# Performance work log

Hardware: AMD Instinct MI355X
Metric: run time of the kernel (lower is better)

Reference implementation:

```python
import jax, jax.numpy as jnp
import numpy as np

N_CODES = 8192
CODE_DIM = 256
COMMITMENT_COST = 0.25
EMA_DECAY = 0.99
EPS = 1e-5


def setup_inputs() -> dict:
    key = jax.random.key(0)
    k1, k2 = jax.random.split(key)
    B, N, D, K = 8, 2048, CODE_DIM, N_CODES
    z = jax.random.normal(k1, (B, N, D), dtype=jnp.float32)
    # torch init: uniform(-1/n_codes, 1/n_codes); use small-scale init for realism
    emb_weight = jax.random.uniform(k2, (K, D), minval=-1.0 / K, maxval=1.0 / K, dtype=jnp.float32)
    return {
        "z": z,
        "emb_weight": emb_weight,
        "ema_cluster_size": jnp.zeros((K,), jnp.float32),
        "ema_w": jnp.zeros((K, D), jnp.float32),
        "code_usage": jnp.zeros((K,), jnp.float32),
    }


def reference(z, emb_weight, ema_cluster_size, ema_w, code_usage):
    # training=True path of VectorQuantizerV2.forward
    B, N, D = z.shape
    K = emb_weight.shape[0]
    z_flat = z.reshape(-1, D)  # [T, D], T = B*N

    # squared L2 distances: ||z||^2 + ||e||^2 - 2 z e^T  -> [T, K]
    d = (jnp.sum(z_flat * z_flat, axis=1, keepdims=True)
         + jnp.sum(emb_weight * emb_weight, axis=1)
         - 2.0 * z_flat @ emb_weight.T)
    idx = jnp.argmin(d, axis=-1)  # [T] int32

    z_q = emb_weight[idx].reshape(B, N, D)

    # usage tracking (scatter-add of ones == segment counts)
    cluster_size = jax.ops.segment_sum(jnp.ones_like(idx, jnp.float32), idx, num_segments=K)
    new_code_usage = code_usage + cluster_size

    # EMA codebook update (no one-hot materialization; segment_sum == encodings.T @ z)
    new_ecs = ema_cluster_size * EMA_DECAY + (1.0 - EMA_DECAY) * cluster_size
    n = jnp.sum(new_ecs)
    new_ecs = (new_ecs + EPS) / (n + K * EPS) * n  # Laplace smoothing
    dw = jax.ops.segment_sum(z_flat, idx, num_segments=K)  # [K, D]
    new_ema_w = ema_w * EMA_DECAY + (1.0 - EMA_DECAY) * dw
    new_emb_weight = new_ema_w / jnp.clip(new_ecs, EPS, None)[:, None]

    # losses (computed with z_q from the OLD codebook, matching torch op order)
    commitment_loss = jnp.mean((z - jax.lax.stop_gradient(z_q)) ** 2)
    codebook_loss = jnp.mean((z_q - jax.lax.stop_gradient(z)) ** 2)
    vq_loss = COMMITMENT_COST * commitment_loss + codebook_loss

    # straight-through estimator
    z_q_out = z + jax.lax.stop_gradient(z_q - z)

    # perplexity from empirical code distribution of this batch
    avg_probs = cluster_size / (B * N)
    perplexity = jnp.exp(-jnp.sum(avg_probs * jnp.log(avg_probs + 1e-10)))

    unique_codes = jnp.sum(new_code_usage > 0).astype(jnp.float32)
    usage_ratio = unique_codes / K

    indices = idx.reshape(B, N)
    return (z_q_out, indices, vq_loss, perplexity, usage_ratio, unique_codes,
            new_emb_weight, new_ecs, new_ema_w, new_code_usage)
```

## Files before the change

kernel.cpp:

```cpp
#include <hip/hip_runtime.h>
#include <hip/hip_bf16.h>
#include <math.h>

#define TOKS 16384
#define DDIM 256
#define KC   8192

static constexpr float EMA   = 0.99f;
static constexpr float ONE_M = (float)(1.0 - 0.99);
static constexpr float EPSF  = 1e-5f;
static constexpr float KEPS  = (float)(8192 * 1e-5);

#define CTILE  32
#define CAP    128
#define DELTA  2.0e-4f

#define CS_OFF    0
#define SCAL_OFF  8192
#define AN_OFF    8208
#define BN_OFF    24592
#define IDX_OFF   32784
#define CNT_OFF   49168
#define GMX_OFF   65552
#define THR0_OFF  81936
#define EB_OFF    98320
#define LISTS_OFF 1146896

typedef __attribute__((ext_vector_type(8))) short bf16x8;
typedef __attribute__((ext_vector_type(4))) short bf16x4;
typedef __attribute__((ext_vector_type(4))) float f32x4;

static __device__ inline short f2b(float f) {
  __hip_bfloat16 h = __float2bfloat16(f);
  return *reinterpret_cast<short*>(&h);
}
static __device__ inline unsigned int fkey(float f) {
  unsigned int b = __float_as_uint(f);
  return (b & 0x80000000u) ? ~b : (b | 0x80000000u);
}
static __device__ inline float funkey(unsigned int k) {
  unsigned int b = (k & 0x80000000u) ? (k & 0x7FFFFFFFu) : ~k;
  return __uint_as_float(b);
}

__global__ __launch_bounds__(256) void k_convbn(const float* __restrict__ e,
                                                unsigned short* __restrict__ eb,
                                                float* __restrict__ bn) {
  const int lane = threadIdx.x & 63;
  const int row = blockIdx.x * 4 + (threadIdx.x >> 6);
  const float4 v = *reinterpret_cast<const float4*>(e + (size_t)row * DDIM + lane * 4);
  bf16x4 b;
  b[0] = f2b(v.x); b[1] = f2b(v.y); b[2] = f2b(v.z); b[3] = f2b(v.w);
  *reinterpret_cast<bf16x4*>(eb + (size_t)row * DDIM + lane * 4) = b;
  float s = v.x * v.x + v.y * v.y + v.z * v.z + v.w * v.w;
#pragma unroll
  for (int d = 32; d; d >>= 1) s += __shfl_down(s, d);
  if (lane == 0) bn[row] = s;
}

__global__ __launch_bounds__(256) void k_convz(const float* __restrict__ z,
                                               unsigned short* __restrict__ zb,
                                               float* __restrict__ an) {
  const int lane = threadIdx.x & 63;
  const int row = blockIdx.x * 4 + (threadIdx.x >> 6);
  const float4 v = *reinterpret_cast<const float4*>(z + (size_t)row * DDIM + lane * 4);
  bf16x4 b;
  b[0] = f2b(v.x); b[1] = f2b(v.y); b[2] = f2b(v.z); b[3] = f2b(v.w);
  *reinterpret_cast<bf16x4*>(zb + (size_t)row * DDIM + lane * 4) = b;
  float s = v.x * v.x + v.y * v.y + v.z * v.z + v.w * v.w;
#pragma unroll
  for (int d = 32; d; d >>= 1) s += __shfl_down(s, d);
  if (lane == 0) an[row] = s;
}

template<bool COLLECT>
__global__ __launch_bounds__(256, 4) void k_screen(
    const unsigned short* __restrict__ zb, const unsigned short* __restrict__ eb,
    unsigned int* __restrict__ gmx, const float* __restrict__ thr0,
    unsigned int* __restrict__ cnt, unsigned short* __restrict__ lists) {
  constexpr int CHUNKC = COLLECT ? 1024 : 256;
  constexpr int NITC = CHUNKC / CTILE;
  __shared__ unsigned short Bt[2][CTILE * 256];

  const int tid = threadIdx.x;
  const int lane = tid & 63;
  const int w = tid >> 6;
  const int t0 = blockIdx.x * 128;
  const int k0 = blockIdx.y * CHUNKC;

  bf16x8 a[2][8];
  {
    const int rlo = lane & 15;
    const int khi = (lane >> 4) * 8;
#pragma unroll
    for (int rf = 0; rf < 2; ++rf) {
      const unsigned short* zr =
          zb + (size_t)(t0 + w * 32 + rf * 16 + rlo) * DDIM + khi;
#pragma unroll
      for (int kk = 0; kk < 8; ++kk)
        a[rf][kk] = *reinterpret_cast<const bf16x8*>(zr + kk * 32);
    }
  }

  float tr[2][4];
  float rm[2][4];
#pragma unroll
  for (int rf = 0; rf < 2; ++rf)
#pragma unroll
    for (int r = 0; r < 4; ++r) {
      rm[rf][r] = -1e30f;
      if (COLLECT) tr[rf][r] = thr0[t0 + w * 32 + rf * 16 + (lane >> 4) * 4 + r];
    }

  const char* ebB = reinterpret_cast<const char*>(eb);
  const int sc = tid >> 3;
  const int ss = tid & 7;
  const int swz = (sc & 7) << 4;

  {
    const size_t gb = (size_t)(k0 + sc) * 512 + ss * 16;
    char* dst = reinterpret_cast<char*>(&Bt[0][0]) + sc * 512;
#pragma unroll
    for (int q = 0; q < 4; ++q) {
      const uint4 g = *reinterpret_cast<const uint4*>(ebB + gb + q * 128);
      *reinterpret_cast<uint4*>(dst + ((ss * 16 + q * 128) ^ swz)) = g;
    }
  }
  __syncthreads();

  const int rdlo = lane & 15;
  const int rdhi = (lane >> 4) * 16;
  uint4 g[4];

  for (int ct = 0; ct < NITC; ++ct) {
    if (ct + 1 < NITC) {
      const size_t gb = (size_t)(k0 + (ct + 1) * CTILE + sc) * 512 + ss * 16;
#pragma unroll
      for (int q = 0; q < 4; ++q)
        g[q] = *reinterpret_cast<const uint4*>(ebB + gb + q * 128);
    }

    f32x4 acc[2][2];
#pragma unroll
    for (int rf = 0; rf < 2; ++rf)
#pragma unroll
      for (int cf = 0; cf < 2; ++cf) acc[rf][cf] = (f32x4){0.f, 0.f, 0.f, 0.f};

    const char* buf = reinterpret_cast<const char*>(&Bt[ct & 1][0]);
#pragma unroll
    for (int kk = 0; kk < 8; ++kk) {
      const int off = (kk * 64 + rdhi) ^ ((rdlo & 7) << 4);
      const bf16x8 b0 = *reinterpret_cast<const bf16x8*>(buf + rdlo * 512 + off);
      const bf16x8 b1 = *reinterpret_cast<const bf16x8*>(buf + (16 + rdlo) * 512 + off);
      acc[0][0] = __builtin_amdgcn_mfma_f32_16x16x32_bf16(a[0][kk], b0, acc[0][0], 0, 0, 0);
      acc[1][0] = __builtin_amdgcn_mfma_f32_16x16x32_bf16(a[1][kk], b0, acc[1][0], 0, 0, 0);
      acc[0][1] = __builtin_amdgcn_mfma_f32_16x16x32_bf16(a[0][kk], b1, acc[0][1], 0, 0, 0);
      acc[1][1] = __builtin_amdgcn_mfma_f32_16x16x32_bf16(a[1][kk], b1, acc[1][1], 0, 0, 0);
    }

    if (!COLLECT) {
#pragma unroll
      for (int rf = 0; rf < 2; ++rf)
#pragma unroll
        for (int r = 0; r < 4; ++r)
          rm[rf][r] = fmaxf(rm[rf][r], fmaxf(acc[rf][0][r], acc[rf][1][r]));
    } else {
      const int kb = k0 + ct * CTILE;
#pragma unroll
      for (int rf = 0; rf < 2; ++rf) {
#pragma unroll
        for (int r = 0; r < 4; ++r) {
          const float th = tr[rf][r];
          if (acc[rf][0][r] >= th || acc[rf][1][r] >= th) {
            const int t = t0 + w * 32 + rf * 16 + (lane >> 4) * 4 + r;
            if (acc[rf][0][r] >= th) {
              const unsigned int o_ = atomicAdd(&cnt[t], 1u);
              if (o_ < CAP) lists[(size_t)t * CAP + o_] = (unsigned short)(kb + rdlo);
            }
            if (acc[rf][1][r] >= th) {
              const unsigned int o_ = atomicAdd(&cnt[t], 1u);
              if (o_ < CAP) lists[(size_t)t * CAP + o_] = (unsigned short)(kb + 16 + rdlo);
            }
          }
        }
      }
    }

    if (ct + 1 < NITC) {
      char* dst = reinterpret_cast<char*>(&Bt[(ct + 1) & 1][0]) + sc * 512;
#pragma unroll
      for (int q = 0; q < 4; ++q)
        *reinterpret_cast<uint4*>(dst + ((ss * 16 + q * 128) ^ swz)) = g[q];
    }
    __syncthreads();
  }

  if (!COLLECT) {
#pragma unroll
    for (int rf = 0; rf < 2; ++rf) {
#pragma unroll
      for (int r = 0; r < 4; ++r) {
        float v = rm[rf][r];
#pragma unroll
        for (int o = 1; o <= 8; o <<= 1) v = fmaxf(v, __shfl_xor(v, o));
        if ((lane & 15) == 0) {
          const int t = t0 + w * 32 + rf * 16 + (lane >> 4) * 4 + r;
          atomicMax(&gmx[t], fkey(v));
        }
      }
    }
  }
}

__global__ __launch_bounds__(256) void k_thr(const unsigned int* __restrict__ gmx,
                                             float* __restrict__ thr) {
  const int t = blockIdx.x * 256 + threadIdx.x;
  thr[t] = funkey(gmx[t]) - DELTA;
}

__global__ __launch_bounds__(256) void k_rescore(
    const float* __restrict__ z, const float* __restrict__ emb,
    const float* __restrict__ an, const float* __restrict__ bn,
    const unsigned int* __restrict__ cnt, const unsigned short* __restrict__ lists,
    float* __restrict__ out_idx, int* __restrict__ idx_i) {
  const int w = threadIdx.x >> 6;
  const int lane = threadIdx.x & 63;
  const int t = blockIdx.x * 4 + w;

  const float4 z4 = *reinterpret_cast<const float4*>(z + (size_t)t * DDIM + lane * 4);
  const unsigned int nraw = cnt[t];
  const float aN = an[t];
  float bd = 3.4e38f;
  int bk = 0x7fffffff;

  if (nraw <= CAP) {
    const int n = (int)nraw;
    for (int c = 0; c < n; ++c) {
      const int k = (int)lists[(size_t)t * CAP + c];
      const float4 e4 = *reinterpret_cast<const float4*>(emb + (size_t)k * DDIM + lane * 4);
      float p = z4.x * e4.x + z4.y * e4.y + z4.z * e4.z + z4.w * e4.w;
#pragma unroll
      for (int o = 32; o; o >>= 1) p += __shfl_xor(p, o);
      const float d = __fsub_rn(__fadd_rn(aN, bn[k]), __fmul_rn(2.0f, p));
      if (d < bd || (d == bd && k < bk)) { bd = d; bk = k; }
    }
  } else {
    for (int kb = 0; kb < KC; kb += 4) {
      float p0, p1, p2, p3;
      {
        const float4 e0 = *reinterpret_cast<const float4*>(emb + (size_t)(kb + 0) * DDIM + lane * 4);
        const float4 e1 = *reinterpret_cast<const float4*>(emb + (size_t)(kb + 1) * DDIM + lane * 4);
        const float4 e2 = *reinterpret_cast<const float4*>(emb + (size_t)(kb + 2) * DDIM + lane * 4);
        const float4 e3 = *reinterpret_cast<const float4*>(emb + (size_t)(kb + 3) * DDIM + lane * 4);
        p0 = z4.x * e0.x + z4.y * e0.y + z4.z * e0.z + z4.w * e0.w;
        p1 = z4.x * e1.x + z4.y * e1.y + z4.z * e1.z + z4.w * e1.w;
        p2 = z4.x * e2.x + z4.y * e2.y + z4.z * e2.z + z4.w * e2.w;
        p3 = z4.x * e3.x + z4.y * e3.y + z4.z * e3.z + z4.w * e3.w;
      }
#pragma unroll
      for (int o = 32; o; o >>= 1) {
        p0 += __shfl_xor(p0, o);
        p1 += __shfl_xor(p1, o);
        p2 += __shfl_xor(p2, o);
        p3 += __shfl_xor(p3, o);
      }
      const float d0 = __fsub_rn(__fadd_rn(aN, bn[kb + 0]), __fmul_rn(2.0f, p0));
      const float d1 = __fsub_rn(__fadd_rn(aN, bn[kb + 1]), __fmul_rn(2.0f, p1));
      const float d2 = __fsub_rn(__fadd_rn(aN, bn[kb + 2]), __fmul_rn(2.0f, p2));
      const float d3 = __fsub_rn(__fadd_rn(aN, bn[kb + 3]), __fmul_rn(2.0f, p3));
      if (d0 < bd) { bd = d0; bk = kb + 0; }
      if (d1 < bd) { bd = d1; bk = kb + 1; }
      if (d2 < bd) { bd = d2; bk = kb + 2; }
      if (d3 < bd) { bd = d3; bk = kb + 3; }
    }
  }

  if (lane == 0) { out_idx[t] = (float)bk; idx_i[t] = bk; }
}

__global__ __launch_bounds__(256) void k_scale_ema(const float* __restrict__ ema_w,
                                                   float* __restrict__ o8) {
  const size_t i = ((size_t)blockIdx.x * 256 + threadIdx.x) * 4;
  const float4 v = *reinterpret_cast<const float4*>(ema_w + i);
  float4 r;
  r.x = EMA * v.x; r.y = EMA * v.y; r.z = EMA * v.z; r.w = EMA * v.w;
  *reinterpret_cast<float4*>(o8 + i) = r;
}

__global__ __launch_bounds__(256) void k_quant(const float* __restrict__ z,
                                               const float* __restrict__ emb,
                                               const int* __restrict__ idx_i,
                                               float* __restrict__ o0,
                                               float* __restrict__ o8,
                                               float* __restrict__ cs,
                                               float* __restrict__ scal) {
  const int w = threadIdx.x >> 6;
  const int lane = threadIdx.x & 63;
  const int tb = blockIdx.x * 16 + w * 4;
  float lsum = 0.f;

#pragma unroll
  for (int i = 0; i < 4; ++i) {
    const int t = tb + i;
    const int k = idx_i[t];
    const float4 zv = *reinterpret_cast<const float4*>(z + (size_t)t * DDIM + lane * 4);
    const float4 ev = *reinterpret_cast<const float4*>(emb + (size_t)k * DDIM + lane * 4);
    float4 o;
    o.x = __fadd_rn(zv.x, __fsub_rn(ev.x, zv.x));
    o.y = __fadd_rn(zv.y, __fsub_rn(ev.y, zv.y));
    o.z = __fadd_rn(zv.z, __fsub_rn(ev.z, zv.z));
    o.w = __fadd_rn(zv.w, __fsub_rn(ev.w, zv.w));
    *reinterpret_cast<float4*>(o0 + (size_t)t * DDIM + lane * 4) = o;
    const float dx = __fsub_rn(zv.x, ev.x);
    const float dy = __fsub_rn(zv.y, ev.y);
    const float dz = __fsub_rn(zv.z, ev.z);
    const float dw = __fsub_rn(zv.w, ev.w);
    lsum += dx * dx + dy * dy + dz * dz + dw * dw;
    float* dst = o8 + (size_t)k * DDIM + lane * 4;
    unsafeAtomicAdd(dst + 0, ONE_M * zv.x);
    unsafeAtomicAdd(dst + 1, ONE_M * zv.y);
    unsafeAtomicAdd(dst + 2, ONE_M * zv.z);
    unsafeAtomicAdd(dst + 3, ONE_M * zv.w);
    if (lane == 0) atomicAdd(cs + k, 1.0f);
  }

#pragma unroll
  for (int o = 32; o; o >>= 1) lsum += __shfl_down(lsum, o);
  __shared__ float wsum[4];
  if (lane == 0) wsum[w] = lsum;
  __syncthreads();
  if (threadIdx.x == 0)
    atomicAdd(scal + 0, wsum[0] + wsum[1] + wsum[2] + wsum[3]);
}

__global__ __launch_bounds__(256) void k_stats(const float* __restrict__ ecs_in,
                                               const float* __restrict__ cu_in,
                                               const float* __restrict__ cs,
                                               float* __restrict__ o7,
                                               float* __restrict__ o9,
                                               float* __restrict__ scal) {
  const int k = blockIdx.x * 256 + threadIdx.x;
  const int w = threadIdx.x >> 6;
  const int lane = threadIdx.x & 63;
  const float cc = cs[k];
  const float raw = EMA * ecs_in[k] + ONE_M * cc;
  o7[k] = raw;
  const float ncu = __fadd_rn(cu_in[k], cc);
  o9[k] = ncu;
  const float p = cc * (1.0f / 16384.0f);
  float s0 = raw;
  float s1 = p * logf(p + 1e-10f);
  float s2 = ncu > 0.0f ? 1.0f : 0.0f;
#pragma unroll
  for (int o = 32; o; o >>= 1) {
    s0 += __shfl_down(s0, o);
    s1 += __shfl_down(s1, o);
    s2 += __shfl_down(s2, o);
  }
  __shared__ float w0[4], w1[4], w2[4];
  if (lane == 0) { w0[w] = s0; w1[w] = s1; w2[w] = s2; }
  __syncthreads();
  if (threadIdx.x == 0) {
    atomicAdd(scal + 1, w0[0] + w0[1] + w0[2] + w0[3]);
    atomicAdd(scal + 2, w1[0] + w1[1] + w1[2] + w1[3]);
    atomicAdd(scal + 3, w2[0] + w2[1] + w2[2] + w2[3]);
  }
}

__global__ __launch_bounds__(256) void k_final(float* __restrict__ o7,
                                               const float* __restrict__ o8,
                                               const float* __restrict__ scal,
                                               float* __restrict__ o6,
                                               float* __restrict__ o2,
                                               float* __restrict__ o3,
                                               float* __restrict__ o4,
                                               float* __restrict__ o5) {
  const int lane = threadIdx.x & 63;
  const int k = blockIdx.x * 4 + (threadIdx.x >> 6);
  const float n = scal[1];
  const float raw = o7[k];
  const float sm = (raw + EPSF) / (n + KEPS) * n;
  if (lane == 0) o7[k] = sm;
  const float dnm = fmaxf(sm, EPSF);
  const size_t i = (size_t)k * DDIM + lane * 4;
  const float4 v = *reinterpret_cast<const float4*>(o8 + i);
  float4 r;
  r.x = v.x / dnm; r.y = v.y / dnm; r.z = v.z / dnm; r.w = v.w / dnm;
  *reinterpret_cast<float4*>(o6 + i) = r;
  if (blockIdx.x == 0 && threadIdx.x == 0) {
    const float m = scal[0] * (1.0f / 4194304.0f);
    o2[0] = 0.25f * m + m;
    o3[0] = expf(-scal[2]);
    o4[0] = scal[3] * (1.0f / 8192.0f);
    o5[0] = scal[3];
  }
}

extern "C" void kernel_launch(void* const* d_in, const int* in_sizes, int n_in,
                              void* d_out, int out_size, void* d_ws, size_t ws_size,
                              hipStream_t stream) {
  const float* z     = (const float*)d_in[0];
  const float* emb   = (const float*)d_in[1];
  const float* ecs   = (const float*)d_in[2];
  const float* ema_w = (const float*)d_in[3];
  const float* cu    = (const float*)d_in[4];

  float* out = (float*)d_out;
  float* o0 = out;
  float* o1 = o0 + 4194304;
  float* o2 = o1 + 16384;
  float* o3 = o2 + 1;
  float* o4 = o3 + 1;
  float* o5 = o4 + 1;
  float* o6 = o5 + 1;
  float* o7 = o6 + 2097152;
  float* o8 = o7 + 8192;
  float* o9 = o8 + 2097152;

  float* w    = (float*)d_ws;
  float* cs   = w + CS_OFF;
  float* scal = w + SCAL_OFF;
  float* an   = w + AN_OFF;
  float* bn   = w + BN_OFF;
  int*   idxi = (int*)(w + IDX_OFF);
  unsigned int* cnt = (unsigned int*)(w + CNT_OFF);
  unsigned int* gmx = (unsigned int*)(w + GMX_OFF);
  float* thr0 = w + THR0_OFF;
  unsigned short* eb = (unsigned short*)(w + EB_OFF);
  unsigned short* lists = (unsigned short*)(w + LISTS_OFF);
  unsigned short* zb = (unsigned short*)o0;

  hipMemsetAsync(w + CS_OFF, 0, (8192 + 16) * sizeof(float), stream);
  hipMemsetAsync(w + CNT_OFF, 0, 2 * TOKS * sizeof(unsigned int), stream);

  k_convbn<<<KC / 4, 256, 0, stream>>>(emb, eb, bn);
  k_convz<<<TOKS / 4, 256, 0, stream>>>(z, zb, an);

  k_screen<false><<<dim3(TOKS / 128, 8), 256, 0, stream>>>(zb, eb, gmx, thr0, cnt, lists);
  k_thr<<<TOKS / 256, 256, 0, stream>>>(gmx, thr0);
  k_screen<true><<<dim3(TOKS / 128, 8), 256, 0, stream>>>(zb, eb, gmx, thr0, cnt, lists);
  k_rescore<<<TOKS / 4, 256, 0, stream>>>(z, emb, an, bn, cnt, lists, o1, idxi);

  k_scale_ema<<<(KC * DDIM) / 1024, 256, 0, stream>>>(ema_w, o8);
  k_quant<<<TOKS / 16, 256, 0, stream>>>(z, emb, idxi, o0, o8, cs, scal);

  k_stats<<<KC / 256, 256, 0, stream>>>(ecs, cu, cs, o7, o9, scal);
  k_final<<<KC / 4, 256, 0, stream>>>(o7, o8, scal, o6, o2, o3, o4, o5);
}
```

Before: 277.7 us.

## Fuse conversion kernels, inline threshold computation, merge quantize into rescore

New measurement: 266.2 us. 4.1% less time.

```diff
diff --git a/kernel.cpp b/kernel.cpp
--- a/kernel.cpp
+++ b/kernel.cpp
@@ -19,12 +19,12 @@
 #define SCAL_OFF  8192
 #define AN_OFF    8208
 #define BN_OFF    24592
-#define IDX_OFF   32784
-#define CNT_OFF   49168
-#define GMX_OFF   65552
-#define THR0_OFF  81936
-#define EB_OFF    98320
-#define LISTS_OFF 1146896
+#define CNT_OFF   41?
+#undef CNT_OFF
+#define CNT_OFF   32784
+#define GMX_OFF   49168
+#define EB_OFF    65552
+#define LISTS_OFF 1114128
 
 typedef __attribute__((ext_vector_type(8))) short bf16x8;
 typedef __attribute__((ext_vector_type(4))) short bf16x4;
@@ -43,40 +43,33 @@
   return __uint_as_float(b);
 }
 
-__global__ __launch_bounds__(256) void k_convbn(const float* __restrict__ e,
-                                                unsigned short* __restrict__ eb,
-                                                float* __restrict__ bn) {
+__global__ __launch_bounds__(256) void k_conv(const float* __restrict__ e,
+                                              const float* __restrict__ z,
+                                              unsigned short* __restrict__ eb,
+                                              unsigned short* __restrict__ zb,
+                                              float* __restrict__ bn,
+                                              float* __restrict__ an) {
   const int lane = threadIdx.x & 63;
   const int row = blockIdx.x * 4 + (threadIdx.x >> 6);
-  const float4 v = *reinterpret_cast<const float4*>(e + (size_t)row * DDIM + lane * 4);
+  const bool isE = row < KC;
+  const float* src = isE ? e : z;
+  unsigned short* dst = isE ? eb : zb;
+  float* nrm = isE ? bn : an;
+  const int r = isE ? row : row - KC;
+  const float4 v = *reinterpret_cast<const float4*>(src + (size_t)r * DDIM + lane * 4);
   bf16x4 b;
   b[0] = f2b(v.x); b[1] = f2b(v.y); b[2] = f2b(v.z); b[3] = f2b(v.w);
-  *reinterpret_cast<bf16x4*>(eb + (size_t)row * DDIM + lane * 4) = b;
+  *reinterpret_cast<bf16x4*>(dst + (size_t)r * DDIM + lane * 4) = b;
   float s = v.x * v.x + v.y * v.y + v.z * v.z + v.w * v.w;
 #pragma unroll
   for (int d = 32; d; d >>= 1) s += __shfl_down(s, d);
-  if (lane == 0) bn[row] = s;
-}
-
-__global__ __launch_bounds__(256) void k_convz(const float* __restrict__ z,
-                                               unsigned short* __restrict__ zb,
-                                               float* __restrict__ an) {
-  const int lane = threadIdx.x & 63;
-  const int row = blockIdx.x * 4 + (threadIdx.x >> 6);
-  const float4 v = *reinterpret_cast<const float4*>(z + (size_t)row * DDIM + lane * 4);
-  bf16x4 b;
-  b[0] = f2b(v.x); b[1] = f2b(v.y); b[2] = f2b(v.z); b[3] = f2b(v.w);
-  *reinterpret_cast<bf16x4*>(zb + (size_t)row * DDIM + lane * 4) = b;
-  float s = v.x * v.x + v.y * v.y + v.z * v.z + v.w * v.w;
-#pragma unroll
-  for (int d = 32; d; d >>= 1) s += __shfl_down(s, d);
-  if (lane == 0) an[row] = s;
+  if (lane == 0) nrm[r] = s;
 }
 
 template<bool COLLECT>
 __global__ __launch_bounds__(256, 4) void k_screen(
     const unsigned short* __restrict__ zb, const unsigned short* __restrict__ eb,
-    unsigned int* __restrict__ gmx, const float* __restrict__ thr0,
+    unsigned int* __restrict__ gmx,
     unsigned int* __restrict__ cnt, unsigned short* __restrict__ lists) {
   constexpr int CHUNKC = COLLECT ? 1024 : 256;
   constexpr int NITC = CHUNKC / CTILE;
@@ -109,7 +102,8 @@
 #pragma unroll
     for (int r = 0; r < 4; ++r) {
       rm[rf][r] = -1e30f;
-      if (COLLECT) tr[rf][r] = thr0[t0 + w * 32 + rf * 16 + (lane >> 4) * 4 + r];
+      if (COLLECT)
+        tr[rf][r] = funkey(gmx[t0 + w * 32 + rf * 16 + (lane >> 4) * 4 + r]) - DELTA;
     }
 
   const char* ebB = reinterpret_cast<const char*>(eb);
@@ -212,17 +206,12 @@
   }
 }
 
-__global__ __launch_bounds__(256) void k_thr(const unsigned int* __restrict__ gmx,
-                                             float* __restrict__ thr) {
-  const int t = blockIdx.x * 256 + threadIdx.x;
-  thr[t] = funkey(gmx[t]) - DELTA;
-}
-
 __global__ __launch_bounds__(256) void k_rescore(
     const float* __restrict__ z, const float* __restrict__ emb,
     const float* __restrict__ an, const float* __restrict__ bn,
     const unsigned int* __restrict__ cnt, const unsigned short* __restrict__ lists,
-    float* __restrict__ out_idx, int* __restrict__ idx_i) {
+    float* __restrict__ out_idx, float* __restrict__ o0,
+    float* __restrict__ o8, float* __restrict__ cs, float* __restrict__ scal) {
   const int w = threadIdx.x >> 6;
   const int lane = threadIdx.x & 63;
   const int t = blockIdx.x * 4 + w;
@@ -275,7 +264,34 @@
     }
   }
 
-  if (lane == 0) { out_idx[t] = (float)bk; idx_i[t] = bk; }
+  if (lane == 0) out_idx[t] = (float)bk;
+
+  const float4 ev = *reinterpret_cast<const float4*>(emb + (size_t)bk * DDIM + lane * 4);
+  float4 o;
+  o.x = __fadd_rn(z4.x, __fsub_rn(ev.x, z4.x));
+  o.y = __fadd_rn(z4.y, __fsub_rn(ev.y, z4.y));
+  o.z = __fadd_rn(z4.z, __fsub_rn(ev.z, z4.z));
+  o.w = __fadd_rn(z4.w, __fsub_rn(ev.w, z4.w));
+  *reinterpret_cast<float4*>(o0 + (size_t)t * DDIM + lane * 4) = o;
+  const float dx = __fsub_rn(z4.x, ev.x);
+  const float dy = __fsub_rn(z4.y, ev.y);
+  const float dz = __fsub_rn(z4.z, ev.z);
+  const float dw = __fsub_rn(z4.w, ev.w);
+  float lsum = dx * dx + dy * dy + dz * dz + dw * dw;
+  float* dst = o8 + (size_t)bk * DDIM + lane * 4;
+  unsafeAtomicAdd(dst + 0, ONE_M * z4.x);
+  unsafeAtomicAdd(dst + 1, ONE_M * z4.y);
+  unsafeAtomicAdd(dst + 2, ONE_M * z4.z);
+  unsafeAtomicAdd(dst + 3, ONE_M * z4.w);
+  if (lane == 0) atomicAdd(cs + bk, 1.0f);
+
+#pragma unroll
+  for (int o_ = 32; o_; o_ >>= 1) lsum += __shfl_down(lsum, o_);
+  __shared__ float wsum[4];
+  if (lane == 0) wsum[w] = lsum;
+  __syncthreads();
+  if (threadIdx.x == 0)
+    atomicAdd(scal + 0, wsum[0] + wsum[1] + wsum[2] + wsum[3]);
 }
 
 __global__ __launch_bounds__(256) void k_scale_ema(const float* __restrict__ ema_w,
@@ -285,52 +301,6 @@
   float4 r;
   r.x = EMA * v.x; r.y = EMA * v.y; r.z = EMA * v.z; r.w = EMA * v.w;
   *reinterpret_cast<float4*>(o8 + i) = r;
-}
-
-__global__ __launch_bounds__(256) void k_quant(const float* __restrict__ z,
-                                               const float* __restrict__ emb,
-                                               const int* __restrict__ idx_i,
-                                               float* __restrict__ o0,
-                                               float* __restrict__ o8,
-                                               float* __restrict__ cs,
-                                               float* __restrict__ scal) {
-  const int w = threadIdx.x >> 6;
-  const int lane = threadIdx.x & 63;
-  const int tb = blockIdx.x * 16 + w * 4;
-  float lsum = 0.f;
-
-#pragma unroll
-  for (int i = 0; i < 4; ++i) {
-    const int t = tb + i;
-    const int k = idx_i[t];
-    const float4 zv = *reinterpret_cast<const float4*>(z + (size_t)t * DDIM + lane * 4);
-    const float4 ev = *reinterpret_cast<const float4*>(emb + (size_t)k * DDIM + lane * 4);
-    float4 o;
-    o.x = __fadd_rn(zv.x, __fsub_rn(ev.x, zv.x));
-    o.y = __fadd_rn(zv.y, __fsub_rn(ev.y, zv.y));
-    o.z = __fadd_rn(zv.z, __fsub_rn(ev.z, zv.z));
-    o.w = __fadd_rn(zv.w, __fsub_rn(ev.w, zv.w));
-    *reinterpret_cast<float4*>(o0 + (size_t)t * DDIM + lane * 4) = o;
-    const float dx = __fsub_rn(zv.x, ev.x);
-    const float dy = __fsub_rn(zv.y, ev.y);
-    const float dz = __fsub_rn(zv.z, ev.z);
-    const float dw = __fsub_rn(zv.w, ev.w);
-    lsum += dx * dx + dy * dy + dz * dz + dw * dw;
-    float* dst = o8 + (size_t)k * DDIM + lane * 4;
-    unsafeAtomicAdd(dst + 0, ONE_M * zv.x);
-    unsafeAtomicAdd(dst + 1, ONE_M * zv.y);
-    unsafeAtomicAdd(dst + 2, ONE_M * zv.z);
-    unsafeAtomicAdd(dst + 3, ONE_M * zv.w);
-    if (lane == 0) atomicAdd(cs + k, 1.0f);
-  }
-
-#pragma unroll
-  for (int o = 32; o; o >>= 1) lsum += __shfl_down(lsum, o);
-  __shared__ float wsum[4];
-  if (lane == 0) wsum[w] = lsum;
-  __syncthreads();
-  if (threadIdx.x == 0)
-    atomicAdd(scal + 0, wsum[0] + wsum[1] + wsum[2] + wsum[3]);
 }
 
 __global__ __launch_bounds__(256) void k_stats(const float* __restrict__ ecs_in,
@@ -422,10 +392,8 @@
   float* scal = w + SCAL_OFF;
   float* an   = w + AN_OFF;
   float* bn   = w + BN_OFF;
-  int*   idxi = (int*)(w + IDX_OFF);
   unsigned int* cnt = (unsigned int*)(w + CNT_OFF);
   unsigned int* gmx = (unsigned int*)(w + GMX_OFF);
-  float* thr0 = w + THR0_OFF;
   unsigned short* eb = (unsigned short*)(w + EB_OFF);
   unsigned short* lists = (unsigned short*)(w + LISTS_OFF);
   unsigned short* zb = (unsigned short*)o0;
@@ -433,16 +401,13 @@
   hipMemsetAsync(w + CS_OFF, 0, (8192 + 16) * sizeof(float), stream);
   hipMemsetAsync(w + CNT_OFF, 0, 2 * TOKS * sizeof(unsigned int), stream);
 
-  k_convbn<<<KC / 4, 256, 0, stream>>>(emb, eb, bn);
-  k_convz<<<TOKS / 4, 256, 0, stream>>>(z, zb, an);
-
-  k_screen<false><<<dim3(TOKS / 128, 8), 256, 0, stream>>>(zb, eb, gmx, thr0, cnt, lists);
-  k_thr<<<TOKS / 256, 256, 0, stream>>>(gmx, thr0);
-  k_screen<true><<<dim3(TOKS / 128, 8), 256, 0, stream>>>(zb, eb, gmx, thr0, cnt, lists);
-  k_rescore<<<TOKS / 4, 256, 0, stream>>>(z, emb, an, bn, cnt, lists, o1, idxi);
+  k_conv<<<(KC + TOKS) / 4, 256, 0, stream>>>(emb, z, eb, zb, bn, an);
+
+  k_screen<false><<<dim3(TOKS / 128, 8), 256, 0, stream>>>(zb, eb, gmx, cnt, lists);
+  k_screen<true><<<dim3(TOKS / 128, 8), 256, 0, stream>>>(zb, eb, gmx, cnt, lists);
 
   k_scale_ema<<<(KC * DDIM) / 1024, 256, 0, stream>>>(ema_w, o8);
-  k_quant<<<TOKS / 16, 256, 0, stream>>>(z, emb, idxi, o0, o8, cs, scal);
+  k_rescore<<<TOKS / 4, 256, 0, stream>>>(z, emb, an, bn, cnt, lists, o1, o0, o8, cs, scal);
 
   k_stats<<<KC / 256, 256, 0, stream>>>(ecs, cu, cs, o7, o9, scal);
   k_final<<<KC / 4, 256, 0, stream>>>(o7, o8, scal, o6, o2, o3, o4, o5);
```
